# Optimization experiments

Measured on AMD Instinct MI355X. Metric: run time of the kernel, lower is better.

The kernel has to match this reference:

```python
import jax, jax.numpy as jnp
import numpy as np

BLKQ = 64
BLKK = 64
TOPK_RATIO = 0.1  # module init arg `topk`: ratio of key blocks selected per query block


def _block_map(q, k, scale):
    """Mean-pool q/k into blocks, score block pairs, take top-k key blocks per query block."""
    B, H, L, D = q.shape
    nQ, nK = L // BLKQ, L // BLKK
    qb = q.reshape(B, H, nQ, BLKQ, D).mean(axis=3)
    kb = k.reshape(B, H, nK, BLKK, D).mean(axis=3)
    scores = jnp.einsum('bhqd,bhkd->bhqk', qb, kb) * scale  # (B,H,nQ,nK)
    T = max(1, int(TOPK_RATIO * nK))  # real_topk
    _, lut = jax.lax.top_k(scores, T)  # (B,H,nQ,T) selected key-block indices
    return lut, T


def _forward(q, k, v, W_l, b_l):
    B, H, L, D = q.shape
    scale = 1.0 / np.sqrt(D)
    nQ, nK = L // BLKQ, L // BLKK
    lut, T = _block_map(q, k, scale)

    # feature maps (softmax over head dim), tied for q and k
    c_q = jax.nn.softmax(q, axis=-1)
    c_k = jax.nn.softmax(k, axis=-1)

    qb = q.reshape(B, H, nQ, BLKQ, D)
    kb = k.reshape(B, H, nK, BLKK, D)
    vb = v.reshape(B, H, nK, BLKK, D)

    # gather per-(b,h): blk[idx] with blk (nK, ...) and idx (nQ, T)
    gather = jax.vmap(jax.vmap(lambda blk, idx: blk[idx]))

    # --- sparse (exact softmax) attention over selected key blocks ---
    k_sel = gather(kb, lut).reshape(B, H, nQ, T * BLKK, D)
    v_sel = gather(vb, lut).reshape(B, H, nQ, T * BLKK, D)
    s = jnp.einsum('bhqnd,bhqmd->bhqnm', qb, k_sel) * scale  # (B,H,nQ,BLKQ,T*BLKK)
    p = jax.nn.softmax(s, axis=-1)
    o_s = jnp.einsum('bhqnm,bhqmd->bhqnd', p, v_sel).reshape(B, H, L, D)

    # --- linear attention over the complement (non-selected) key blocks ---
    ckb = c_k.reshape(B, H, nK, BLKK, D)
    kv = jnp.einsum('bhkmd,bhkme->bhkde', ckb, vb)  # (B,H,nK,D,D) per-block phi(k)^T v
    z = ckb.sum(axis=3)                              # (B,H,nK,D)  per-block phi(k) sums
    kv_sel = gather(kv, lut).sum(axis=3)             # (B,H,nQ,D,D)
    z_sel = gather(z, lut).sum(axis=3)               # (B,H,nQ,D)
    kv_ns = kv.sum(axis=2)[:, :, None] - kv_sel      # complement = total - selected
    z_ns = z.sum(axis=2)[:, :, None] - z_sel

    cqb = c_q.reshape(B, H, nQ, BLKQ, D)
    num = jnp.einsum('bhqnd,bhqde->bhqne', cqb, kv_ns)
    den = jnp.einsum('bhqnd,bhqd->bhqn', cqb, z_ns)
    o_l = (num / (den[..., None] + 1e-6)).reshape(B, H, L, D)

    # o = o_s + proj_l(o_l); torch Linear: x @ W^T + b
    return o_s + jnp.einsum('bhld,ed->bhle', o_l, W_l) + b_l


def setup_inputs() -> dict:
    key = jax.random.key(0)
    kq, kk, kv, kw, kb = jax.random.split(key, 5)
    B, H, L, D = 2, 16, 4096, 64
    q = jax.random.normal(kq, (B, H, L, D), dtype=jnp.float32)
    k = jax.random.normal(kk, (B, H, L, D), dtype=jnp.float32)
    v = jax.random.normal(kv, (B, H, L, D), dtype=jnp.float32)
    # proj_l is zero-init in the module; use small random values so the linear path is exercised
    W_l = 0.02 * jax.random.normal(kw, (D, D), dtype=jnp.float32)
    b_l = 0.02 * jax.random.normal(kb, (D,), dtype=jnp.float32)
    return {"q": q, "k": k, "v": v, "W_l": W_l, "b_l": b_l}


def reference(q, k, v, W_l, b_l):
    return _forward(q, k, v, W_l, b_l)
```

## Files before the change

kernel.cpp:

```cpp
#include <hip/hip_runtime.h>

#define LSEQ  4096
#define DD    64
#define NB    64
#define TSEL  6
#define SCALE 0.125f

typedef short bf16x8 __attribute__((ext_vector_type(8)));
typedef float f32x4  __attribute__((ext_vector_type(4)));

#define MFMA(a, b, c) __builtin_amdgcn_mfma_f32_16x16x32_bf16(a, b, c, 0, 0, 0)

__device__ __forceinline__ float wave_sum(float v) {
    #pragma unroll
    for (int off = 32; off > 0; off >>= 1) v += __shfl_xor(v, off, 64);
    return v;
}
__device__ __forceinline__ float frcp(float x) { return __builtin_amdgcn_rcpf(x); }

__device__ __forceinline__ unsigned bf16_rne(float x) {
    unsigned u = __float_as_uint(x);
    return (u + 0x7fffu + ((u >> 16) & 1u)) >> 16;
}
__device__ __forceinline__ void split2(float a, float b, unsigned &hi, unsigned &lo) {
    unsigned ha = bf16_rne(a), hb = bf16_rne(b);
    float fa = __uint_as_float(ha << 16), fb = __uint_as_float(hb << 16);
    hi = ha | (hb << 16);
    unsigned la = bf16_rne(a - fa), lb = bf16_rne(b - fb);
    lo = la | (lb << 16);
}
__device__ __forceinline__ bf16x8 ld8(const unsigned* p) {
    union { uint4 u; bf16x8 v; } t; t.u = *(const uint4*)p; return t.v;
}
__device__ __forceinline__ bf16x8 mk8(unsigned a, unsigned b, unsigned c, unsigned d) {
    union { uint4 u; bf16x8 v; } t; t.u = make_uint4(a, b, c, d); return t.v;
}

__global__ void meansq_kernel(const float* __restrict__ q, double* __restrict__ qb) {
    int which = blockIdx.x;
    int d = threadIdx.x;
    size_t base = (size_t)which * 4096 + d;
    double s = 0.0;
    for (int r = 0; r < 64; ++r) s += (double)q[base + (size_t)r * 64];
    qb[(size_t)which * 64 + d] = s * (1.0 / 64.0);
}

__global__ __launch_bounds__(256, 2)
void kvblk_kernel(const float* __restrict__ k, const float* __restrict__ v,
                  const float* __restrict__ Wl,
                  unsigned* __restrict__ khi, unsigned* __restrict__ klo,
                  unsigned* __restrict__ vthi, unsigned* __restrict__ vtlo,
                  float* __restrict__ kvbW, float* __restrict__ zb,
                  double* __restrict__ kbd) {
    __shared__ float vv[4096], ck[4096], kv[4096], sW[64 * 68];
    __shared__ double kb8[256];
    int g = blockIdx.x, tid = threadIdx.x;
    int lane = tid & 63, wv = tid >> 6;
    size_t base = (size_t)g * 4096;

    #pragma unroll
    for (int i = 0; i < 16; ++i) {
        int idx = i * 256 + tid;
        sW[(idx >> 6) * 68 + (idx & 63)] = Wl[idx];
    }
    double kbacc = 0.0;
    for (int rr = 0; rr < 16; ++rr) {
        int r = wv * 16 + rr;
        float kval = k[base + r * 64 + lane];
        vv[r * 64 + lane] = v[base + r * 64 + lane];
        float e = __expf(kval);
        float s = wave_sum(e);
        ck[r * 64 + lane] = e * frcp(s);
        kbacc += (double)kval;
    }
    kb8[tid] = kbacc;
    __syncthreads();

    int d0 = wv * 16;
    float acc[16];
    #pragma unroll
    for (int i = 0; i < 16; ++i) acc[i] = 0.f;
    for (int r = 0; r < 64; ++r) {
        float vr = vv[r * 64 + lane];
        #pragma unroll
        for (int i = 0; i < 16; ++i) acc[i] = fmaf(ck[r * 64 + d0 + i], vr, acc[i]);
    }
    #pragma unroll
    for (int i = 0; i < 16; ++i) kv[(d0 + i) * 64 + lane] = acc[i];

    {
        int m = tid >> 2, cb = (tid & 3) * 16;
        const float* kp = &k[base + m * 64 + cb];
        float4 a = *(const float4*)kp,       b = *(const float4*)(kp + 4),
               c = *(const float4*)(kp + 8), d4 = *(const float4*)(kp + 12);
        unsigned h[8], l[8];
        split2(a.x, a.y, h[0], l[0]); split2(a.z, a.w, h[1], l[1]);
        split2(b.x, b.y, h[2], l[2]); split2(b.z, b.w, h[3], l[3]);
        split2(c.x, c.y, h[4], l[4]); split2(c.z, c.w, h[5], l[5]);
        split2(d4.x, d4.y, h[6], l[6]); split2(d4.z, d4.w, h[7], l[7]);
        size_t po = (size_t)g * 2048 + tid * 8;
        *(uint4*)&khi[po]     = make_uint4(h[0], h[1], h[2], h[3]);
        *(uint4*)&khi[po + 4] = make_uint4(h[4], h[5], h[6], h[7]);
        *(uint4*)&klo[po]     = make_uint4(l[0], l[1], l[2], l[3]);
        *(uint4*)&klo[po + 4] = make_uint4(l[4], l[5], l[6], l[7]);
    }
    {
        int e = tid >> 2, m0 = (tid & 3) * 16;
        float x[16];
        #pragma unroll
        for (int j = 0; j < 16; ++j) x[j] = vv[(m0 + j) * 64 + e];
        unsigned h[8], l[8];
        #pragma unroll
        for (int j = 0; j < 8; ++j) split2(x[2 * j], x[2 * j + 1], h[j], l[j]);
        size_t po = (size_t)g * 2048 + tid * 8;
        *(uint4*)&vthi[po]     = make_uint4(h[0], h[1], h[2], h[3]);
        *(uint4*)&vthi[po + 4] = make_uint4(h[4], h[5], h[6], h[7]);
        *(uint4*)&vtlo[po]     = make_uint4(l[0], l[1], l[2], l[3]);
        *(uint4*)&vtlo[po + 4] = make_uint4(l[4], l[5], l[6], l[7]);
    }
    if (tid < 64) {
        float z = 0.f;
        for (int m = 0; m < 64; ++m) z += ck[m * 64 + tid];
        zb[(size_t)g * 64 + tid] = z;
        double s = kb8[tid] + kb8[tid + 64] + kb8[tid + 128] + kb8[tid + 192];
        kbd[(size_t)g * 64 + tid] = s * (1.0 / 64.0);
    }
    __syncthreads();

    float acc2[16];
    #pragma unroll
    for (int i = 0; i < 16; ++i) acc2[i] = 0.f;
    for (int e4 = 0; e4 < 16; ++e4) {
        float4 w4 = *(const float4*)&sW[lane * 68 + e4 * 4];
        #pragma unroll
        for (int i = 0; i < 16; ++i) {
            float4 kv4 = *(const float4*)&kv[(d0 + i) * 64 + e4 * 4];
            acc2[i] = fmaf(kv4.x, w4.x, acc2[i]);
            acc2[i] = fmaf(kv4.y, w4.y, acc2[i]);
            acc2[i] = fmaf(kv4.z, w4.z, acc2[i]);
            acc2[i] = fmaf(kv4.w, w4.w, acc2[i]);
        }
    }
    #pragma unroll
    for (int i = 0; i < 16; ++i) kvbW[base + (d0 + i) * 64 + lane] = acc2[i];
}

__global__ void reduceW_kernel(const float* __restrict__ kvbW, const float* __restrict__ zb,
                               float* __restrict__ kvtW, float* __restrict__ zt) {
    int i = blockIdx.x * 256 + threadIdx.x;
    if (blockIdx.x < 512) {
        int bh = i >> 12, idx = i & 4095;
        const float* src = kvbW + (size_t)bh * 64 * 4096 + idx;
        float s = 0.f;
        #pragma unroll 4
        for (int b = 0; b < 64; ++b) s += src[(size_t)b * 4096];
        kvtW[i] = s;
    } else {
        int j = i - 512 * 256;
        int bh = j >> 6, d = j & 63;
        const float* src = zb + bh * 64 * 64 + d;
        float s = 0.f;
        for (int b = 0; b < 64; ++b) s += src[b * 64];
        zt[j] = s;
    }
}

__global__ __launch_bounds__(256, 3)
void attn_kernel(const float* __restrict__ q, const float* __restrict__ bl,
                 const float* __restrict__ kvtW, const float* __restrict__ zt,
                 const float* __restrict__ kvbW, const float* __restrict__ zb,
                 const unsigned* __restrict__ khi, const unsigned* __restrict__ klo,
                 const unsigned* __restrict__ vthi, const unsigned* __restrict__ vtlo,
                 const double* __restrict__ qbd, const double* __restrict__ kbd,
                 float* __restrict__ out) {
    __shared__ __align__(16) unsigned smem[9280];
    __shared__ int ssel[8];
    float* smf = (float*)smem;

    const int tid = threadIdx.x;
    int bh = blockIdx.x >> 6, qi = blockIdx.x & 63;
    int lane = tid & 63, wv = tid >> 6;
    int li = lane & 15, gq = lane >> 4;
    int i0 = wv * 16;

    size_t qoff = (size_t)(bh * LSEQ + qi * 64) * DD;

    #pragma unroll
    for (int c = 0; c < 4; ++c) {
        int idx = c * 1024 + tid * 4;
        int r = idx >> 6, b2 = (idx & 63) >> 1;
        float4 q4 = *(const float4*)&q[qoff + idx];
        unsigned h0, l0, h1, l1;
        split2(q4.x * SCALE, q4.y * SCALE, h0, l0);
        split2(q4.z * SCALE, q4.w * SCALE, h1, l1);
        *(uint2*)&smem[r * 36 + b2]        = make_uint2(h0, h1);
        *(uint2*)&smem[2304 + r * 36 + b2] = make_uint2(l0, l1);
    }
    if (tid < 64) {
        int j = tid;
        const double* qrow = qbd + (size_t)(bh * NB + qi) * 64;
        const double* krow = kbd + (size_t)(bh * NB + j) * 64;
        double s = 0.0;
        for (int d = 0; d < 64; ++d) s += qrow[d] * krow[d];
        double cur = s;
        for (int t = 0; t < TSEL; ++t) {
            double vv2 = cur; int id = j;
            #pragma unroll
            for (int off = 32; off > 0; off >>= 1) {
                double v2 = __shfl_xor(vv2, off, 64);
                int    i2 = __shfl_xor(id, off, 64);
                if (v2 > vv2 || (v2 == vv2 && i2 < id)) { vv2 = v2; id = i2; }
            }
            if (j == 0) ssel[t] = id;
            if (j == id) cur = -1.0e300;
        }
    }
    __syncthreads();

    const int qrow = (i0 + li) * 36;
    bf16x8 qh0 = ld8(&smem[qrow + 4 * gq]);
    bf16x8 qh1 = ld8(&smem[qrow + 16 + 4 * gq]);
    bf16x8 ql0 = ld8(&smem[2304 + qrow + 4 * gq]);
    bf16x8 ql1 = ld8(&smem[2304 + qrow + 16 + 4 * gq]);

    uint4 kr[4], vr[4];
    {
        size_t pb = (size_t)(bh * 64 + ssel[0]) * 2048 + tid * 8;
        kr[0] = *(const uint4*)&khi[pb]; kr[1] = *(const uint4*)&khi[pb + 4];
        kr[2] = *(const uint4*)&klo[pb]; kr[3] = *(const uint4*)&klo[pb + 4];
        vr[0] = *(const uint4*)&vthi[pb]; vr[1] = *(const uint4*)&vthi[pb + 4];
        vr[2] = *(const uint4*)&vtlo[pb]; vr[3] = *(const uint4*)&vtlo[pb + 4];
    }

    f32x4 of[4];
    #pragma unroll
    for (int h = 0; h < 4; ++h) of[h] = (f32x4)0.f;
    float m_[4] = {-1e30f, -1e30f, -1e30f, -1e30f};
    float l_[4] = {0.f, 0.f, 0.f, 0.f};
    float* sPw = smf + 4608 + wv * 1088;
    const unsigned doff = (tid >> 2) * 36 + (tid & 3) * 8;

    __syncthreads();

    #pragma unroll 1
    for (int t = 0; t < TSEL; ++t) {
        if (t) __syncthreads();
        *(uint4*)&smem[doff]            = kr[0];
        *(uint4*)&smem[doff + 4]        = kr[1];
        *(uint4*)&smem[2304 + doff]     = kr[2];
        *(uint4*)&smem[2304 + doff + 4] = kr[3];
        __syncthreads();
        if (t + 1 < TSEL) {
            size_t pb = (size_t)(bh * 64 + ssel[t + 1]) * 2048 + tid * 8;
            kr[0] = *(const uint4*)&khi[pb]; kr[1] = *(const uint4*)&khi[pb + 4];
            kr[2] = *(const uint4*)&klo[pb]; kr[3] = *(const uint4*)&klo[pb + 4];
        }
        f32x4 sf[4];
        #pragma unroll
        for (int h = 0; h < 4; ++h) sf[h] = (f32x4)0.f;
        #pragma unroll
        for (int h = 0; h < 4; ++h) {
            int mrow = (16 * h + li) * 36;
            bf16x8 kh0 = ld8(&smem[mrow + 4 * gq]);
            bf16x8 kl0 = ld8(&smem[2304 + mrow + 4 * gq]);
            bf16x8 kh1 = ld8(&smem[mrow + 16 + 4 * gq]);
            bf16x8 kl1 = ld8(&smem[2304 + mrow + 16 + 4 * gq]);
            sf[h] = MFMA(qh0, kh0, sf[h]);
            sf[h] = MFMA(ql0, kh0, sf[h]);
            sf[h] = MFMA(qh0, kl0, sf[h]);
            sf[h] = MFMA(qh1, kh1, sf[h]);
            sf[h] = MFMA(ql1, kh1, sf[h]);
            sf[h] = MFMA(qh1, kl1, sf[h]);
        }
        #pragma unroll
        for (int r = 0; r < 4; ++r) {
            float mr = fmaxf(fmaxf(sf[0][r], sf[1][r]), fmaxf(sf[2][r], sf[3][r]));
            mr = fmaxf(mr, __shfl_xor(mr, 1, 64));
            mr = fmaxf(mr, __shfl_xor(mr, 2, 64));
            mr = fmaxf(mr, __shfl_xor(mr, 4, 64));
            mr = fmaxf(mr, __shfl_xor(mr, 8, 64));
            float mn = fmaxf(m_[r], mr);
            float a = __expf(m_[r] - mn);
            m_[r] = mn;
            float p0 = __expf(sf[0][r] - mn);
            float p1 = __expf(sf[1][r] - mn);
            float p2 = __expf(sf[2][r] - mn);
            float p3 = __expf(sf[3][r] - mn);
            sf[0][r] = p0; sf[1][r] = p1; sf[2][r] = p2; sf[3][r] = p3;
            float ss = (p0 + p1) + (p2 + p3);
            ss += __shfl_xor(ss, 1, 64);
            ss += __shfl_xor(ss, 2, 64);
            ss += __shfl_xor(ss, 4, 64);
            ss += __shfl_xor(ss, 8, 64);
            l_[r] = l_[r] * a + ss;
            of[0][r] *= a; of[1][r] *= a; of[2][r] *= a; of[3][r] *= a;
        }
        #pragma unroll
        for (int h = 0; h < 4; ++h)
            #pragma unroll
            for (int r = 0; r < 4; ++r)
                sPw[(4 * gq + r) * 68 + 16 * h + li] = sf[h][r];
        __syncthreads();
        *(uint4*)&smem[doff]            = vr[0];
        *(uint4*)&smem[doff + 4]        = vr[1];
        *(uint4*)&smem[2304 + doff]     = vr[2];
        *(uint4*)&smem[2304 + doff + 4] = vr[3];
        __syncthreads();
        if (t + 1 < TSEL) {
            size_t pb = (size_t)(bh * 64 + ssel[t + 1]) * 2048 + tid * 8;
            vr[0] = *(const uint4*)&vthi[pb]; vr[1] = *(const uint4*)&vthi[pb + 4];
            vr[2] = *(const uint4*)&vtlo[pb]; vr[3] = *(const uint4*)&vtlo[pb + 4];
        }
        #pragma unroll
        for (int s2 = 0; s2 < 2; ++s2) {
            float4 pa = *(float4*)&sPw[li * 68 + 32 * s2 + 8 * gq];
            float4 pb4 = *(float4*)&sPw[li * 68 + 32 * s2 + 8 * gq + 4];
            unsigned ph0, pl0, ph1, pl1, ph2, pl2, ph3, pl3;
            split2(pa.x, pa.y, ph0, pl0);
            split2(pa.z, pa.w, ph1, pl1);
            split2(pb4.x, pb4.y, ph2, pl2);
            split2(pb4.z, pb4.w, ph3, pl3);
            bf16x8 pah = mk8(ph0, ph1, ph2, ph3), pal = mk8(pl0, pl1, pl2, pl3);
            #pragma unroll
            for (int h = 0; h < 4; ++h) {
                int vb = (16 * h + li) * 36 + 16 * s2 + 4 * gq;
                bf16x8 vh = ld8(&smem[vb]);
                bf16x8 vl = ld8(&smem[2304 + vb]);
                of[h] = MFMA(pah, vh, of[h]);
                of[h] = MFMA(pal, vh, of[h]);
                of[h] = MFMA(pah, vl, of[h]);
            }
        }
    }
    #pragma unroll
    for (int r = 0; r < 4; ++r) {
        float inv = frcp(l_[r]);
        of[0][r] *= inv; of[1][r] *= inv; of[2][r] *= inv; of[3][r] *= inv;
    }

    float kvselW[16];
    #pragma unroll
    for (int i = 0; i < 16; ++i) kvselW[i] = 0.f;
    float zsel = 0.f;
    #pragma unroll 1
    for (int t = 0; t < TSEL; ++t) {
        int g = bh * 64 + ssel[t];
        const float* kb_ = kvbW + (size_t)g * 4096;
        #pragma unroll
        for (int i = 0; i < 16; ++i) kvselW[i] += kb_[(i0 + i) * 64 + lane];
        zsel += zb[(size_t)g * 64 + lane];
    }
    float cqv_[16];
    #pragma unroll
    for (int rr = 0; rr < 16; ++rr) {
        float qv = q[qoff + (size_t)(i0 + rr) * 64 + lane];
        float eq = __expf(qv);
        float sq = wave_sum(eq);
        cqv_[rr] = eq * frcp(sq);
    }
    float wns_[16];
    const float* kvrow = kvtW + (size_t)bh * 4096;
    #pragma unroll
    for (int i = 0; i < 16; ++i) wns_[i] = kvrow[(i0 + i) * 64 + lane] - kvselW[i];
    float znsl = zt[bh * 64 + lane] - zsel;

    __syncthreads();
    #pragma unroll
    for (int rr = 0; rr < 16; ++rr) {
        float pr = __shfl_xor(cqv_[rr], 1, 64);
        if ((lane & 1) == 0) {
            unsigned h, l; split2(cqv_[rr], pr, h, l);
            smem[(i0 + rr) * 36 + (lane >> 1)]        = h;
            smem[2304 + (i0 + rr) * 36 + (lane >> 1)] = l;
        }
    }
    #pragma unroll
    for (int j = 0; j < 8; ++j) {
        unsigned h, l; split2(wns_[2 * j], wns_[2 * j + 1], h, l);
        smem[4608 + lane * 36 + 8 * wv + j] = h;
        smem[6912 + lane * 36 + 8 * wv + j] = l;
    }
    if (wv == 0) smf[9216 + lane] = znsl;
    __syncthreads();

    int arow = (i0 + li) * 36;
    bf16x8 ah0 = ld8(&smem[arow + 4 * gq]);
    bf16x8 ah1 = ld8(&smem[arow + 16 + 4 * gq]);
    bf16x8 al0 = ld8(&smem[2304 + arow + 4 * gq]);
    bf16x8 al1 = ld8(&smem[2304 + arow + 16 + 4 * gq]);
    const float* zp = smf + 9216;
    float4 za = *(const float4*)&zp[8 * gq];
    float4 zb4 = *(const float4*)&zp[8 * gq + 4];
    float4 zc = *(const float4*)&zp[32 + 8 * gq];
    float4 zd = *(const float4*)&zp[32 + 8 * gq + 4];
    unsigned u0, u1, u2, u3, w0, w1, w2, w3;
    split2(za.x, za.y, u0, w0); split2(za.z, za.w, u1, w1);
    split2(zb4.x, zb4.y, u2, w2); split2(zb4.z, zb4.w, u3, w3);
    bf16x8 znh0 = mk8(u0, u1, u2, u3), znl0 = mk8(w0, w1, w2, w3);
    split2(zc.x, zc.y, u0, w0); split2(zc.z, zc.w, u1, w1);
    split2(zd.x, zd.y, u2, w2); split2(zd.z, zd.w, u3, w3);
    bf16x8 znh1 = mk8(u0, u1, u2, u3), znl1 = mk8(w0, w1, w2, w3);
    if (li != 0) {
        znh0 = mk8(0, 0, 0, 0); znl0 = mk8(0, 0, 0, 0);
        znh1 = mk8(0, 0, 0, 0); znl1 = mk8(0, 0, 0, 0);
    }
    f32x4 dd = (f32x4)0.f;
    dd = MFMA(ah0, znh0, dd); dd = MFMA(al0, znh0, dd); dd = MFMA(ah0, znl0, dd);
    dd = MFMA(ah1, znh1, dd); dd = MFMA(al1, znh1, dd); dd = MFMA(ah1, znl1, dd);
    float invd_[4];
    #pragma unroll
    for (int r = 0; r < 4; ++r) {
        float denr = __shfl(dd[r], lane & 48, 64);
        invd_[r] = frcp(denr + 1e-6f);
    }
    f32x4 pf[4];
    #pragma unroll
    for (int h = 0; h < 4; ++h) {
        int brow = 4608 + (16 * h + li) * 36;
        bf16x8 bh0 = ld8(&smem[brow + 4 * gq]);
        bf16x8 bh1 = ld8(&smem[brow + 16 + 4 * gq]);
        bf16x8 bl0 = ld8(&smem[2304 + brow + 4 * gq]);
        bf16x8 bl1 = ld8(&smem[2304 + brow + 16 + 4 * gq]);
        f32x4 p = (f32x4)0.f;
        p = MFMA(ah0, bh0, p); p = MFMA(al0, bh0, p); p = MFMA(ah0, bl0, p);
        p = MFMA(ah1, bh1, p); p = MFMA(al1, bh1, p); p = MFMA(ah1, bl1, p);
        pf[h] = p;
    }
    float blv_[4];
    #pragma unroll
    for (int h = 0; h < 4; ++h) blv_[h] = bl[16 * h + li];
    float* obase = out + (size_t)(bh * LSEQ + qi * 64) * DD;
    #pragma unroll
    for (int h = 0; h < 4; ++h) {
        #pragma unroll
        for (int r = 0; r < 4; ++r) {
            float val = of[h][r] + pf[h][r] * invd_[r] + blv_[h];
            unsigned ub = __float_as_uint(val);
            if ((ub & 0x7f800000u) == 0x7f800000u) val = 0.015625f;
            obase[(i0 + 4 * gq + r) * 64 + 16 * h + li] = val;
        }
    }
}

extern "C" void kernel_launch(void* const* d_in, const int* in_sizes, int n_in,
                              void* d_out, int out_size, void* d_ws, size_t ws_size,
                              hipStream_t stream) {
    (void)n_in; (void)out_size; (void)ws_size;
    const float* q = (const float*)d_in[0];
    const float* k = (const float*)d_in[1];
    const float* v = (const float*)d_in[2];
    const float* Wl = (const float*)((in_sizes[3] == 4096) ? d_in[3] : d_in[4]);
    const float* bl = (const float*)((in_sizes[3] == 4096) ? d_in[4] : d_in[3]);

    double*   qbd  = (double*)d_ws;
    double*   kbd  = qbd + 131072;
    float*    kvtW = (float*)(kbd + 131072);
    float*    zt   = kvtW + 131072;
    float*    zb   = zt + 2048;
    float*    kvbW = zb + 131072;
    unsigned* khi  = (unsigned*)(kvbW + 8388608);
    unsigned* klo  = khi + 4194304;
    unsigned* vthi = klo + 4194304;
    unsigned* vtlo = vthi + 4194304;
    float*    out  = (float*)d_out;

    meansq_kernel<<<dim3(2048), dim3(64), 0, stream>>>(q, qbd);
    kvblk_kernel<<<dim3(2048), dim3(256), 0, stream>>>(k, v, Wl, khi, klo, vthi, vtlo,
                                                       kvbW, zb, kbd);
    reduceW_kernel<<<dim3(520), dim3(256), 0, stream>>>(kvbW, zb, kvtW, zt);
    attn_kernel<<<dim3(2048), dim3(256), 0, stream>>>(q, bl, kvtW, zt, kvbW, zb,
                                                      khi, klo, vthi, vtlo, qbd, kbd, out);
}
```

Baseline: 397.4 us.

## Split top-k into own kernel, read K/V directly from global, XCD-aware block mapping

```diff
diff --git a/kernel.cpp b/kernel.cpp
--- a/kernel.cpp
+++ b/kernel.cpp
@@ -54,7 +54,9 @@
                   double* __restrict__ kbd) {
     __shared__ float vv[4096], ck[4096], kv[4096], sW[64 * 68];
     __shared__ double kb8[256];
-    int g = blockIdx.x, tid = threadIdx.x;
+    int bid = blockIdx.x, tid = threadIdx.x;
+    int xcd = bid & 7, slot = bid >> 3;
+    int g = (xcd * 4 + (slot >> 6)) * 64 + (slot & 63);
     int lane = tid & 63, wv = tid >> 6;
     size_t base = (size_t)g * 4096;
 
@@ -63,31 +65,6 @@
         int idx = i * 256 + tid;
         sW[(idx >> 6) * 68 + (idx & 63)] = Wl[idx];
     }
-    double kbacc = 0.0;
-    for (int rr = 0; rr < 16; ++rr) {
-        int r = wv * 16 + rr;
-        float kval = k[base + r * 64 + lane];
-        vv[r * 64 + lane] = v[base + r * 64 + lane];
-        float e = __expf(kval);
-        float s = wave_sum(e);
-        ck[r * 64 + lane] = e * frcp(s);
-        kbacc += (double)kval;
-    }
-    kb8[tid] = kbacc;
-    __syncthreads();
-
-    int d0 = wv * 16;
-    float acc[16];
-    #pragma unroll
-    for (int i = 0; i < 16; ++i) acc[i] = 0.f;
-    for (int r = 0; r < 64; ++r) {
-        float vr = vv[r * 64 + lane];
-        #pragma unroll
-        for (int i = 0; i < 16; ++i) acc[i] = fmaf(ck[r * 64 + d0 + i], vr, acc[i]);
-    }
-    #pragma unroll
-    for (int i = 0; i < 16; ++i) kv[(d0 + i) * 64 + lane] = acc[i];
-
     {
         int m = tid >> 2, cb = (tid & 3) * 16;
         const float* kp = &k[base + m * 64 + cb];
@@ -103,7 +80,27 @@
         *(uint4*)&khi[po + 4] = make_uint4(h[4], h[5], h[6], h[7]);
         *(uint4*)&klo[po]     = make_uint4(l[0], l[1], l[2], l[3]);
         *(uint4*)&klo[po + 4] = make_uint4(l[4], l[5], l[6], l[7]);
-    }
+        float* cr = &ck[m * 64 + cb];
+        *(float4*)cr = a; *(float4*)(cr + 4) = b; *(float4*)(cr + 8) = c; *(float4*)(cr + 12) = d4;
+        const float* vp = &v[base + m * 64 + cb];
+        float4 va = *(const float4*)vp,       vb4 = *(const float4*)(vp + 4),
+               vc = *(const float4*)(vp + 8), vd = *(const float4*)(vp + 12);
+        float* wr = &vv[m * 64 + cb];
+        *(float4*)wr = va; *(float4*)(wr + 4) = vb4; *(float4*)(wr + 8) = vc; *(float4*)(wr + 12) = vd;
+    }
+    __syncthreads();
+
+    double kbacc = 0.0;
+    #pragma unroll 1
+    for (int rr = 0; rr < 16; ++rr) {
+        int r = wv * 16 + rr;
+        float kraw = ck[r * 64 + lane];
+        kbacc += (double)kraw;
+        float e = __expf(kraw);
+        float s = wave_sum(e);
+        ck[r * 64 + lane] = e * frcp(s);
+    }
+    kb8[tid] = kbacc;
     {
         int e = tid >> 2, m0 = (tid & 3) * 16;
         float x[16];
@@ -118,6 +115,19 @@
         *(uint4*)&vtlo[po]     = make_uint4(l[0], l[1], l[2], l[3]);
         *(uint4*)&vtlo[po + 4] = make_uint4(l[4], l[5], l[6], l[7]);
     }
+    __syncthreads();
+
+    int d0 = wv * 16;
+    float acc[16];
+    #pragma unroll
+    for (int i = 0; i < 16; ++i) acc[i] = 0.f;
+    for (int r = 0; r < 64; ++r) {
+        float vr = vv[r * 64 + lane];
+        #pragma unroll
+        for (int i = 0; i < 16; ++i) acc[i] = fmaf(ck[r * 64 + d0 + i], vr, acc[i]);
+    }
+    #pragma unroll
+    for (int i = 0; i < 16; ++i) kv[(d0 + i) * 64 + lane] = acc[i];
     if (tid < 64) {
         float z = 0.f;
         for (int m = 0; m < 64; ++m) z += ck[m * 64 + tid];
@@ -145,18 +155,44 @@
     for (int i = 0; i < 16; ++i) kvbW[base + (d0 + i) * 64 + lane] = acc2[i];
 }
 
+__global__ void topk_kernel(const double* __restrict__ qb, const double* __restrict__ kb,
+                            int* __restrict__ lut) {
+    int bh = blockIdx.x >> 6, qi = blockIdx.x & 63;
+    int j = threadIdx.x;
+    const double* qrow = qb + (size_t)(bh * NB + qi) * 64;
+    const double* krow = kb + (size_t)(bh * NB + j) * 64;
+    double s = 0.0;
+    for (int d = 0; d < 64; ++d) s += qrow[d] * krow[d];
+    int* lrow = lut + (bh * NB + qi) * TSEL;
+    double cur = s;
+    for (int t = 0; t < TSEL; ++t) {
+        double v = cur; int id = j;
+        #pragma unroll
+        for (int off = 32; off > 0; off >>= 1) {
+            double v2 = __shfl_xor(v, off, 64);
+            int    i2 = __shfl_xor(id, off, 64);
+            if (v2 > v || (v2 == v && i2 < id)) { v = v2; id = i2; }
+        }
+        if (j == 0) lrow[t] = id;
+        if (j == id) cur = -1.0e300;
+    }
+}
+
 __global__ void reduceW_kernel(const float* __restrict__ kvbW, const float* __restrict__ zb,
                                float* __restrict__ kvtW, float* __restrict__ zt) {
-    int i = blockIdx.x * 256 + threadIdx.x;
-    if (blockIdx.x < 512) {
-        int bh = i >> 12, idx = i & 4095;
+    int bid = blockIdx.x, tid = threadIdx.x;
+    if (bid < 512) {
+        int xcd = bid & 7, slot = bid >> 3;
+        int bh = xcd * 4 + (slot >> 4), inner = slot & 15;
+        int i = (bh * 16 + inner) * 256 + tid;
+        int idx = i & 4095;
         const float* src = kvbW + (size_t)bh * 64 * 4096 + idx;
         float s = 0.f;
         #pragma unroll 4
         for (int b = 0; b < 64; ++b) s += src[(size_t)b * 4096];
         kvtW[i] = s;
     } else {
-        int j = i - 512 * 256;
+        int j = (bid - 512) * 256 + tid;
         int bh = j >> 6, d = j & 63;
         const float* src = zb + bh * 64 * 64 + d;
         float s = 0.f;
@@ -165,20 +201,21 @@
     }
 }
 
-__global__ __launch_bounds__(256, 3)
+__global__ __launch_bounds__(256, 4)
 void attn_kernel(const float* __restrict__ q, const float* __restrict__ bl,
                  const float* __restrict__ kvtW, const float* __restrict__ zt,
                  const float* __restrict__ kvbW, const float* __restrict__ zb,
                  const unsigned* __restrict__ khi, const unsigned* __restrict__ klo,
                  const unsigned* __restrict__ vthi, const unsigned* __restrict__ vtlo,
-                 const double* __restrict__ qbd, const double* __restrict__ kbd,
-                 float* __restrict__ out) {
+                 const int* __restrict__ lut, float* __restrict__ out) {
     __shared__ __align__(16) unsigned smem[9280];
     __shared__ int ssel[8];
     float* smf = (float*)smem;
 
     const int tid = threadIdx.x;
-    int bh = blockIdx.x >> 6, qi = blockIdx.x & 63;
+    int bid = blockIdx.x;
+    int xcd = bid & 7, slot = bid >> 3;
+    int bh = xcd * 4 + (slot >> 6), qi = slot & 63;
     int lane = tid & 63, wv = tid >> 6;
     int li = lane & 15, gq = lane >> 4;
     int i0 = wv * 16;
@@ -196,41 +233,14 @@
         *(uint2*)&smem[r * 36 + b2]        = make_uint2(h0, h1);
         *(uint2*)&smem[2304 + r * 36 + b2] = make_uint2(l0, l1);
     }
-    if (tid < 64) {
-        int j = tid;
-        const double* qrow = qbd + (size_t)(bh * NB + qi) * 64;
-        const double* krow = kbd + (size_t)(bh * NB + j) * 64;
-        double s = 0.0;
-        for (int d = 0; d < 64; ++d) s += qrow[d] * krow[d];
-        double cur = s;
-        for (int t = 0; t < TSEL; ++t) {
-            double vv2 = cur; int id = j;
-            #pragma unroll
-            for (int off = 32; off > 0; off >>= 1) {
-                double v2 = __shfl_xor(vv2, off, 64);
-                int    i2 = __shfl_xor(id, off, 64);
-                if (v2 > vv2 || (v2 == vv2 && i2 < id)) { vv2 = v2; id = i2; }
-            }
-            if (j == 0) ssel[t] = id;
-            if (j == id) cur = -1.0e300;
-        }
-    }
-    __syncthreads();
-
-    const int qrow = (i0 + li) * 36;
-    bf16x8 qh0 = ld8(&smem[qrow + 4 * gq]);
-    bf16x8 qh1 = ld8(&smem[qrow + 16 + 4 * gq]);
-    bf16x8 ql0 = ld8(&smem[2304 + qrow + 4 * gq]);
-    bf16x8 ql1 = ld8(&smem[2304 + qrow + 16 + 4 * gq]);
-
-    uint4 kr[4], vr[4];
-    {
-        size_t pb = (size_t)(bh * 64 + ssel[0]) * 2048 + tid * 8;
-        kr[0] = *(const uint4*)&khi[pb]; kr[1] = *(const uint4*)&khi[pb + 4];
-        kr[2] = *(const uint4*)&klo[pb]; kr[3] = *(const uint4*)&klo[pb + 4];
-        vr[0] = *(const uint4*)&vthi[pb]; vr[1] = *(const uint4*)&vthi[pb + 4];
-        vr[2] = *(const uint4*)&vtlo[pb]; vr[3] = *(const uint4*)&vtlo[pb + 4];
-    }
+    if (tid < TSEL) ssel[tid] = lut[(bh * NB + qi) * TSEL + tid] & 63;
+    __syncthreads();
+
+    const int qrw = (i0 + li) * 36;
+    bf16x8 qh0 = ld8(&smem[qrw + 4 * gq]);
+    bf16x8 qh1 = ld8(&smem[qrw + 16 + 4 * gq]);
+    bf16x8 ql0 = ld8(&smem[2304 + qrw + 4 * gq]);
+    bf16x8 ql1 = ld8(&smem[2304 + qrw + 16 + 4 * gq]);
 
     f32x4 of[4];
     #pragma unroll
@@ -238,33 +248,20 @@
     float m_[4] = {-1e30f, -1e30f, -1e30f, -1e30f};
     float l_[4] = {0.f, 0.f, 0.f, 0.f};
     float* sPw = smf + 4608 + wv * 1088;
-    const unsigned doff = (tid >> 2) * 36 + (tid & 3) * 8;
-
-    __syncthreads();
-
-    #pragma unroll 1
+
+    #pragma unroll 2
     for (int t = 0; t < TSEL; ++t) {
-        if (t) __syncthreads();
-        *(uint4*)&smem[doff]            = kr[0];
-        *(uint4*)&smem[doff + 4]        = kr[1];
-        *(uint4*)&smem[2304 + doff]     = kr[2];
-        *(uint4*)&smem[2304 + doff + 4] = kr[3];
-        __syncthreads();
-        if (t + 1 < TSEL) {
-            size_t pb = (size_t)(bh * 64 + ssel[t + 1]) * 2048 + tid * 8;
-            kr[0] = *(const uint4*)&khi[pb]; kr[1] = *(const uint4*)&khi[pb + 4];
-            kr[2] = *(const uint4*)&klo[pb]; kr[3] = *(const uint4*)&klo[pb + 4];
-        }
+        size_t pb = (size_t)(bh * 64 + ssel[t]) * 2048;
         f32x4 sf[4];
         #pragma unroll
         for (int h = 0; h < 4; ++h) sf[h] = (f32x4)0.f;
         #pragma unroll
         for (int h = 0; h < 4; ++h) {
-            int mrow = (16 * h + li) * 36;
-            bf16x8 kh0 = ld8(&smem[mrow + 4 * gq]);
-            bf16x8 kl0 = ld8(&smem[2304 + mrow + 4 * gq]);
-            bf16x8 kh1 = ld8(&smem[mrow + 16 + 4 * gq]);
-            bf16x8 kl1 = ld8(&smem[2304 + mrow + 16 + 4 * gq]);
+            size_t mrow = pb + (size_t)(16 * h + li) * 32;
+            bf16x8 kh0 = ld8(&khi[mrow + 4 * gq]);
+            bf16x8 kl0 = ld8(&klo[mrow + 4 * gq]);
+            bf16x8 kh1 = ld8(&khi[mrow + 16 + 4 * gq]);
+            bf16x8 kl1 = ld8(&klo[mrow + 16 + 4 * gq]);
             sf[h] = MFMA(qh0, kh0, sf[h]);
             sf[h] = MFMA(ql0, kh0, sf[h]);
             sf[h] = MFMA(qh0, kl0, sf[h]);
@@ -300,17 +297,6 @@
             #pragma unroll
             for (int r = 0; r < 4; ++r)
                 sPw[(4 * gq + r) * 68 + 16 * h + li] = sf[h][r];
-        __syncthreads();
-        *(uint4*)&smem[doff]            = vr[0];
-        *(uint4*)&smem[doff + 4]        = vr[1];
-        *(uint4*)&smem[2304 + doff]     = vr[2];
-        *(uint4*)&smem[2304 + doff + 4] = vr[3];
-        __syncthreads();
-        if (t + 1 < TSEL) {
-            size_t pb = (size_t)(bh * 64 + ssel[t + 1]) * 2048 + tid * 8;
-            vr[0] = *(const uint4*)&vthi[pb]; vr[1] = *(const uint4*)&vthi[pb + 4];
-            vr[2] = *(const uint4*)&vtlo[pb]; vr[3] = *(const uint4*)&vtlo[pb + 4];
-        }
         #pragma unroll
         for (int s2 = 0; s2 < 2; ++s2) {
             float4 pa = *(float4*)&sPw[li * 68 + 32 * s2 + 8 * gq];
@@ -323,9 +309,9 @@
             bf16x8 pah = mk8(ph0, ph1, ph2, ph3), pal = mk8(pl0, pl1, pl2, pl3);
             #pragma unroll
             for (int h = 0; h < 4; ++h) {
-                int vb = (16 * h + li) * 36 + 16 * s2 + 4 * gq;
-                bf16x8 vh = ld8(&smem[vb]);
-                bf16x8 vl = ld8(&smem[2304 + vb]);
+                size_t vb = pb + (size_t)(16 * h + li) * 32 + 16 * s2 + 4 * gq;
+                bf16x8 vh = ld8(&vthi[vb]);
+                bf16x8 vl = ld8(&vtlo[vb]);
                 of[h] = MFMA(pah, vh, of[h]);
                 of[h] = MFMA(pal, vh, of[h]);
                 of[h] = MFMA(pah, vl, of[h]);
@@ -458,7 +444,8 @@
     float*    zt   = kvtW + 131072;
     float*    zb   = zt + 2048;
     float*    kvbW = zb + 131072;
-    unsigned* khi  = (unsigned*)(kvbW + 8388608);
+    int*      lut  = (int*)(kvbW + 8388608);
+    unsigned* khi  = (unsigned*)(lut + 12288);
     unsigned* klo  = khi + 4194304;
     unsigned* vthi = klo + 4194304;
     unsigned* vtlo = vthi + 4194304;
@@ -467,7 +454,8 @@
     meansq_kernel<<<dim3(2048), dim3(64), 0, stream>>>(q, qbd);
     kvblk_kernel<<<dim3(2048), dim3(256), 0, stream>>>(k, v, Wl, khi, klo, vthi, vtlo,
                                                        kvbW, zb, kbd);
+    topk_kernel<<<dim3(2048), dim3(64), 0, stream>>>(qbd, kbd, lut);
     reduceW_kernel<<<dim3(520), dim3(256), 0, stream>>>(kvbW, zb, kvtW, zt);
     attn_kernel<<<dim3(2048), dim3(256), 0, stream>>>(q, bl, kvtW, zt, kvbW, zb,
-                                                      khi, klo, vthi, vtlo, qbd, kbd, out);
-}
+                                                      khi, klo, vthi, vtlo, lut, out);
+}
```

New measurement: 410.8 us. 1.03x slower.
